# Kernel optimization log

Measured on AMD Instinct MI355X. Metric: run time of the kernel, lower is better.

Reference implementation:

```python
import jax, jax.numpy as jnp
import numpy as np

B, T, D, NH = 4, 2048, 1024, 16
HD = D // NH


def setup_inputs() -> dict:
    key = jax.random.key(0)
    ks = jax.random.split(key, 6)
    scale = 0.02
    x = jax.random.normal(ks[0], (B, T, D), dtype=jnp.float32)
    Wr = jax.random.normal(ks[1], (D, D), dtype=jnp.float32) * scale
    Wk = jax.random.normal(ks[2], (D, D), dtype=jnp.float32) * scale
    Wv = jax.random.normal(ks[3], (D, D), dtype=jnp.float32) * scale
    Ww = jax.random.normal(ks[4], (D, D), dtype=jnp.float32) * scale
    Wo = jax.random.normal(ks[5], (D, D), dtype=jnp.float32) * scale
    return {"x": x, "Wr": Wr, "Wk": Wk, "Wv": Wv, "Ww": Ww, "Wo": Wo}


def _rwkv7_forward(x, Wr, Wk, Wv, Ww, Wo):
    b, t, d = x.shape
    nh, hd = NH, d // NH
    # projections (F.linear: x @ W.T), no bias
    r = jax.nn.sigmoid(x @ Wr.T).reshape(b, t, nh, hd)
    k = (x @ Wk.T).reshape(b, t, nh, hd)
    v = (x @ Wv.T).reshape(b, t, nh, hd)
    w = (jax.nn.sigmoid(x @ Ww.T) * 0.99).reshape(b, t, nh, hd)

    def step(state, inp):
        # state: [B, nh, hd_v, hd_k]
        w_t, k_t, v_t, r_t = inp  # each [B, nh, hd]
        state = state * w_t[..., :, None] + v_t[..., :, None] * k_t[..., None, :]
        out_t = r_t * state.sum(-1)  # [B, nh, hd]
        return state, out_t

    seq = (jnp.moveaxis(w, 1, 0), jnp.moveaxis(k, 1, 0),
           jnp.moveaxis(v, 1, 0), jnp.moveaxis(r, 1, 0))  # time-major
    state0 = jnp.zeros((b, nh, hd, hd), dtype=x.dtype)
    _, outs = jax.lax.scan(step, state0, seq)  # [T, B, nh, hd]
    out = jnp.moveaxis(outs, 0, 1).reshape(b, t, d)

    # RMSNorm with eps=None -> torch uses dtype eps
    eps = jnp.asarray(jnp.finfo(out.dtype).eps, out.dtype)
    out = out * jax.lax.rsqrt(jnp.mean(out * out, axis=-1, keepdims=True) + eps)
    return out @ Wo.T


def reference(x, Wr, Wk, Wv, Ww, Wo):
    return _rwkv7_forward(x, Wr, Wk, Wv, Ww, Wo)
```

## Files before the change

### kernel.cpp

```cpp
#include <hip/hip_runtime.h>
#include <hip/hip_bf16.h>
#include <stdint.h>


#define BB 4
#define TT 2048
#define DD 1024
#define NHH 16
#define HDD 64
#define CC 64
#define LL 32
#define NCH 4096

using bf16 = __hip_bfloat16;
typedef __attribute__((ext_vector_type(8))) short bfrag8;
typedef __attribute__((ext_vector_type(4))) float f32x4;

__device__ __forceinline__ void async_ld16(const bf16* g, bf16* l) {
  __builtin_amdgcn_global_load_lds(
      (const __attribute__((address_space(1))) uint32_t*)g,
      (__attribute__((address_space(3))) uint32_t*)l, 16, 0, 0);
}

__device__ __forceinline__ float sigm(float x) { return 1.0f / (1.0f + expf(-x)); }
__device__ __forceinline__ float bf2f(bf16 h) {
  unsigned short u = *reinterpret_cast<unsigned short*>(&h);
  return __uint_as_float((unsigned)u << 16);
}
__device__ __forceinline__ unsigned short f2bfbits(float f) {
  bf16 b = __float2bfloat16(f);
  return *reinterpret_cast<unsigned short*>(&b);
}

__global__ __launch_bounds__(256)
void convert_kernel(const float* __restrict__ x,
                    const float* __restrict__ Wr, const float* __restrict__ Wv,
                    const float* __restrict__ Ww, const float* __restrict__ Wo,
                    bf16* __restrict__ x_c, bf16* __restrict__ W_c)
{
  const long g = (long)blockIdx.x * 256 + threadIdx.x;
  const float* src; bf16* dst; long off4;
  if (g < 2097152) { src = x; dst = x_c; off4 = g; }
  else {
    long gg = g - 2097152;
    int wsel = (int)(gg >> 18);
    off4 = gg & 262143;
    src = (wsel == 0) ? Wr : (wsel == 1) ? Wv : (wsel == 2) ? Ww : Wo;
    dst = W_c + (long)wsel * 1048576;
  }
  float4 f = reinterpret_cast<const float4*>(src)[off4];
  ushort4 pk;
  pk.x = f2bfbits(f.x); pk.y = f2bfbits(f.y);
  pk.z = f2bfbits(f.z); pk.w = f2bfbits(f.w);
  reinterpret_cast<ushort4*>(dst)[off4] = pk;
}

__global__ __launch_bounds__(256)
void wksum_kernel(const float* __restrict__ Wk, float* __restrict__ wks)
{
  const int gid = blockIdx.x * 256 + threadIdx.x;
  const int h = gid >> 10, c = gid & 1023;
  float s = 0.0f;
  for (int j = 0; j < 64; ++j)
    s += Wk[(long)((h << 6) + j) * 1024 + c];
  wks[gid] = s;
}

__device__ __forceinline__ void gemm_mainloop(
    const bf16* __restrict__ A, const bf16* __restrict__ W,
    int blockM, int blockN, bf16* a_sh, bf16* b_sh, f32x4 acc[4][4])
{
  const int tid    = threadIdx.x;
  const int wave   = tid >> 6;
  const int lane   = tid & 63;
  const int lane15 = lane & 15;
  const int quad   = lane >> 4;
  const int waveM  = wave >> 1;
  const int waveN  = wave & 1;
  const int s_row  = (wave << 5) + (lane >> 2);
  const int s_col  = (((lane & 3) ^ ((lane >> 2) & 3)) << 3);

  const bf16* gA = A + ((long)(blockM * 128) + s_row) * 1024 + s_col;
  const bf16* gW = W + ((long)(blockN * 128) + s_row) * 1024 + s_col;
  bf16* la = a_sh + wave * 1024;
  bf16* lb = b_sh + wave * 1024;

  const int sw = (quad ^ (lane15 & 3)) << 3;

  for (int k0 = 0; k0 < 1024; k0 += 32) {
    async_ld16(gA + k0,            la);
    async_ld16(gA + k0 + 16*1024,  la + 512);
    async_ld16(gW + k0,            lb);
    async_ld16(gW + k0 + 16*1024,  lb + 512);
    __syncthreads();
    bfrag8 af[4], bfv[4];
#pragma unroll
    for (int mi = 0; mi < 4; ++mi)
      af[mi] = *reinterpret_cast<const bfrag8*>(a_sh + (waveM*64 + mi*16 + lane15)*32 + sw);
#pragma unroll
    for (int ni = 0; ni < 4; ++ni)
      bfv[ni] = *reinterpret_cast<const bfrag8*>(b_sh + (waveN*64 + ni*16 + lane15)*32 + sw);
#pragma unroll
    for (int mi = 0; mi < 4; ++mi)
#pragma unroll
      for (int ni = 0; ni < 4; ++ni)
        acc[mi][ni] = __builtin_amdgcn_mfma_f32_16x16x32_bf16(af[mi], bfv[ni], acc[mi][ni], 0, 0, 0);
    __syncthreads();
  }
}

__global__ __launch_bounds__(256, 2)
void proj_kernel(const bf16* __restrict__ X, const bf16* __restrict__ W_c,
                 bf16* __restrict__ r_out, bf16* __restrict__ v_out,
                 bf16* __restrict__ w_out)
{
  __shared__ __align__(16) bf16 a_sh[128*32];
  __shared__ __align__(16) bf16 b_sh[128*32];
  const int f  = blockIdx.x;
  const int u  = f & 7;
  const int q  = f >> 3;
  const int n  = q & 7;
  const int p  = q >> 3;
  const int mh = p & 7;
  const int mode = p >> 3;
  const int m  = u + (mh << 3);

  const bf16* W = W_c + (long)mode * 1048576;
  f32x4 acc[4][4] = {};
  gemm_mainloop(X, W, m, n, a_sh, b_sh, acc);

  const int tid = threadIdx.x;
  const int wave = tid >> 6, lane = tid & 63;
  const int lane15 = lane & 15, quad = lane >> 4;
  const int waveM = wave >> 1, waveN = wave & 1;
  const int m_base = m * 128 + waveM * 64;
  const int n_base = n * 128 + waveN * 64;
  bf16* outp = (mode == 0) ? r_out : (mode == 1) ? v_out : w_out;
#pragma unroll
  for (int mi = 0; mi < 4; ++mi)
#pragma unroll
    for (int ni = 0; ni < 4; ++ni)
#pragma unroll
      for (int r = 0; r < 4; ++r) {
        float val = acc[mi][ni][r];
        if (mode == 0) val = sigm(val);
        else if (mode == 2) val = sigm(val) * 0.99f;
        int mm = m_base + mi*16 + quad*4 + r;
        int nn = n_base + ni*16 + lane15;
        outp[(long)mm * DD + nn] = __float2bfloat16(val);
      }
}

__global__ __launch_bounds__(256)
void ksum_kernel(const bf16* __restrict__ X, const float* __restrict__ wks,
                 float* __restrict__ ksum)
{
  __shared__ __align__(8) bf16 xs[DD];
  const int m = blockIdx.x;
  const int tid = threadIdx.x;
  *reinterpret_cast<ushort4*>(xs + tid*4) =
      *reinterpret_cast<const ushort4*>(X + (long)m * DD + tid*4);
  __syncthreads();
  const int wave = tid >> 6, lane = tid & 63;
  const int b = m >> 11, t = m & (TT - 1);
#pragma unroll
  for (int hi = 0; hi < 4; ++hi) {
    const int h = wave * 4 + hi;
    float acc = 0.0f;
#pragma unroll
    for (int i = 0; i < 16; ++i) {
      const int c = lane + (i << 6);
      acc += bf2f(xs[c]) * wks[h * DD + c];
    }
#pragma unroll
    for (int msk = 1; msk <= 32; msk <<= 1) acc += __shfl_xor(acc, msk);
    if (lane == 0) ksum[((long)(b * NHH + h)) * TT + t] = acc;
  }
}

__global__ __launch_bounds__(256)
void scanA_kernel(const bf16* __restrict__ v_buf, const bf16* __restrict__ w_buf,
                  const float* __restrict__ ksum,
                  float* __restrict__ Pbuf, float* __restrict__ Abuf)
{
  __shared__ float ks_sh[128];
  const int bh = blockIdx.x;
  const int b = bh >> 4, h = bh & 15;
  const int tid = threadIdx.x;
  const int i = tid & 63;
  const int cg = tid >> 6;
  const int chunk = blockIdx.y * 4 + cg;
  if (tid < 128) ks_sh[tid] = ksum[(long)bh * TT + blockIdx.y * 128 + tid];
  __syncthreads();
  const long base = (long)b * TT * DD + (long)(chunk * LL) * DD + h * HDD + i;
  float s = 0.0f, P = 1.0f;
#pragma unroll
  for (int j = 0; j < LL; ++j) {
    const long idx = base + (long)j * DD;
    float wv = bf2f(w_buf[idx]);
    float vv = bf2f(v_buf[idx]);
    s = fmaf(wv, s, vv * ks_sh[cg * LL + j]);
    P *= wv;
  }
  const int ch = bh * 64 + i;
  Pbuf[chunk * NCH + ch] = P;
  Abuf[chunk * NCH + ch] = s;
}

__global__ __launch_bounds__(256)
void scanB_kernel(const float* __restrict__ Pbuf, float* __restrict__ Abuf)
{
  const int ch = blockIdx.x * 256 + threadIdx.x;
  float carry = 0.0f;
  for (int c = 0; c < CC; ++c) {
    const int idx = c * NCH + ch;
    float p = Pbuf[idx];
    float a = Abuf[idx];
    Abuf[idx] = carry;
    carry = fmaf(p, carry, a);
  }
}

__global__ __launch_bounds__(256)
void scanC_kernel(const bf16* __restrict__ r_buf, bf16* v_so,
                  const bf16* __restrict__ w_buf, const float* __restrict__ ksum,
                  const float* __restrict__ Abuf)
{
  __shared__ float ks_sh[128];
  const int bh = blockIdx.x;
  const int b = bh >> 4, h = bh & 15;
  const int tid = threadIdx.x;
  const int i = tid & 63;
  const int cg = tid >> 6;
  const int chunk = blockIdx.y * 4 + cg;
  if (tid < 128) ks_sh[tid] = ksum[(long)bh * TT + blockIdx.y * 128 + tid];
  __syncthreads();
  const int ch = bh * 64 + i;
  const long base = (long)b * TT * DD + (long)(chunk * LL) * DD + h * HDD + i;
  float s = Abuf[chunk * NCH + ch];
#pragma unroll
  for (int j = 0; j < LL; ++j) {
    const long idx = base + (long)j * DD;
    float wv = bf2f(w_buf[idx]);
    float vv = bf2f(v_so[idx]);
    float rv = bf2f(r_buf[idx]);
    s = fmaf(wv, s, vv * ks_sh[cg * LL + j]);
    v_so[idx] = __float2bfloat16(rv * s);
  }
}

__global__ __launch_bounds__(256)
void rmsnorm_inplace(bf16* so)
{
  const long row = blockIdx.x;
  bf16* p = so + row * DD + threadIdx.x * 4;
  ushort4 u = *reinterpret_cast<const ushort4*>(p);
  float x0 = __uint_as_float((unsigned)u.x << 16);
  float x1 = __uint_as_float((unsigned)u.y << 16);
  float x2 = __uint_as_float((unsigned)u.z << 16);
  float x3 = __uint_as_float((unsigned)u.w << 16);
  float ss = x0*x0 + x1*x1 + x2*x2 + x3*x3;
#pragma unroll
  for (int m = 1; m <= 32; m <<= 1) ss += __shfl_xor(ss, m);
  __shared__ float part[4];
  if ((threadIdx.x & 63) == 0) part[threadIdx.x >> 6] = ss;
  __syncthreads();
  const float total = part[0] + part[1] + part[2] + part[3];
  const float scale = rsqrtf(total * (1.0f / DD) + 1.1920929e-07f);
  ushort4 pk;
  pk.x = f2bfbits(x0 * scale); pk.y = f2bfbits(x1 * scale);
  pk.z = f2bfbits(x2 * scale); pk.w = f2bfbits(x3 * scale);
  *reinterpret_cast<ushort4*>(p) = pk;
}

__global__ __launch_bounds__(256, 2)
void out_gemm_kernel(const bf16* __restrict__ A, const bf16* __restrict__ Wo_c,
                     float* __restrict__ out)
{
  __shared__ __align__(16) bf16 a_sh[128*32];
  __shared__ __align__(16) bf16 b_sh[128*32];
  const int f  = blockIdx.x;
  const int u  = f & 7;
  const int q  = f >> 3;
  const int n  = q & 7;
  const int mh = q >> 3;
  const int m  = u + (mh << 3);

  f32x4 acc[4][4] = {};
  gemm_mainloop(A, Wo_c, m, n, a_sh, b_sh, acc);

  const int tid = threadIdx.x;
  const int wave = tid >> 6, lane = tid & 63;
  const int lane15 = lane & 15, quad = lane >> 4;
  const int waveM = wave >> 1, waveN = wave & 1;
  const int m_base = m * 128 + waveM * 64;
  const int n_base = n * 128 + waveN * 64;
#pragma unroll
  for (int mi = 0; mi < 4; ++mi)
#pragma unroll
    for (int ni = 0; ni < 4; ++ni)
#pragma unroll
      for (int r = 0; r < 4; ++r) {
        int mm = m_base + mi*16 + quad*4 + r;
        int nn = n_base + ni*16 + lane15;
        out[(long)mm * DD + nn] = acc[mi][ni][r];
      }
}

extern "C" void kernel_launch(void* const* d_in, const int* in_sizes, int n_in,
                              void* d_out, int out_size, void* d_ws, size_t ws_size,
                              hipStream_t stream) {
  const float* x  = (const float*)d_in[0];
  const float* Wr = (const float*)d_in[1];
  const float* Wk = (const float*)d_in[2];
  const float* Wv = (const float*)d_in[3];
  const float* Ww = (const float*)d_in[4];
  const float* Wo = (const float*)d_in[5];

  const long NELT = (long)BB * TT * DD;
  bf16*  x_c  = (bf16*)d_ws;
  bf16*  W_c  = x_c + NELT;
  bf16*  v_so = W_c + 4 * 1048576;
  float* ksum = (float*)(v_so + NELT);
  float* wks  = ksum + (long)BB * NHH * TT;
  float* Pbuf = wks + NHH * DD;
  float* Abuf = Pbuf + (long)CC * NCH;

  bf16*  r_buf = (bf16*)d_out;
  bf16*  w_buf = (bf16*)d_out + NELT;
  float* out   = (float*)d_out;

  convert_kernel<<<dim3(12288), 256, 0, stream>>>(x, Wr, Wv, Ww, Wo, x_c, W_c);
  wksum_kernel<<<dim3(64), 256, 0, stream>>>(Wk, wks);
  proj_kernel<<<dim3(1536), 256, 0, stream>>>(x_c, W_c, r_buf, v_so, w_buf);
  ksum_kernel<<<dim3(BB * TT), 256, 0, stream>>>(x_c, wks, ksum);
  scanA_kernel<<<dim3(64, 16), 256, 0, stream>>>(v_so, w_buf, ksum, Pbuf, Abuf);
  scanB_kernel<<<dim3(16), 256, 0, stream>>>(Pbuf, Abuf);
  scanC_kernel<<<dim3(64, 16), 256, 0, stream>>>(r_buf, v_so, w_buf, ksum, Abuf);
  rmsnorm_inplace<<<dim3(BB * TT), 256, 0, stream>>>(v_so);
  out_gemm_kernel<<<dim3(512), 256, 0, stream>>>(v_so, W_c + 3 * 1048576, out);
}
```

Before: 266.0 us.

## Double GEMM K-tile to 64, fuse wksum into convert, use fast sigmoid

```diff
diff --git a/kernel.cpp b/kernel.cpp
--- a/kernel.cpp
+++ b/kernel.cpp
@@ -22,7 +22,9 @@
       (__attribute__((address_space(3))) uint32_t*)l, 16, 0, 0);
 }
 
-__device__ __forceinline__ float sigm(float x) { return 1.0f / (1.0f + expf(-x)); }
+__device__ __forceinline__ float sigm(float x) {
+  return __builtin_amdgcn_rcpf(1.0f + __expf(-x));
+}
 __device__ __forceinline__ float bf2f(bf16 h) {
   unsigned short u = *reinterpret_cast<unsigned short*>(&h);
   return __uint_as_float((unsigned)u << 16);
@@ -36,8 +38,19 @@
 void convert_kernel(const float* __restrict__ x,
                     const float* __restrict__ Wr, const float* __restrict__ Wv,
                     const float* __restrict__ Ww, const float* __restrict__ Wo,
-                    bf16* __restrict__ x_c, bf16* __restrict__ W_c)
-{
+                    const float* __restrict__ Wk,
+                    bf16* __restrict__ x_c, bf16* __restrict__ W_c,
+                    float* __restrict__ wks)
+{
+  if (blockIdx.x >= 12288) {
+    const int gid = (blockIdx.x - 12288) * 256 + threadIdx.x;
+    const int h = gid >> 10, c = gid & 1023;
+    float s = 0.0f;
+    for (int j = 0; j < 64; ++j)
+      s += Wk[(long)((h << 6) + j) * 1024 + c];
+    wks[gid] = s;
+    return;
+  }
   const long g = (long)blockIdx.x * 256 + threadIdx.x;
   const float* src; bf16* dst; long off4;
   if (g < 2097152) { src = x; dst = x_c; off4 = g; }
@@ -55,17 +68,6 @@
   reinterpret_cast<ushort4*>(dst)[off4] = pk;
 }
 
-__global__ __launch_bounds__(256)
-void wksum_kernel(const float* __restrict__ Wk, float* __restrict__ wks)
-{
-  const int gid = blockIdx.x * 256 + threadIdx.x;
-  const int h = gid >> 10, c = gid & 1023;
-  float s = 0.0f;
-  for (int j = 0; j < 64; ++j)
-    s += Wk[(long)((h << 6) + j) * 1024 + c];
-  wks[gid] = s;
-}
-
 __device__ __forceinline__ void gemm_mainloop(
     const bf16* __restrict__ A, const bf16* __restrict__ W,
     int blockM, int blockN, bf16* a_sh, bf16* b_sh, f32x4 acc[4][4])
@@ -77,34 +79,39 @@
   const int quad   = lane >> 4;
   const int waveM  = wave >> 1;
   const int waveN  = wave & 1;
-  const int s_row  = (wave << 5) + (lane >> 2);
-  const int s_col  = (((lane & 3) ^ ((lane >> 2) & 3)) << 3);
+  const int s_row  = (wave << 5) + (lane >> 3);
+  const int s_col  = (((lane & 7) ^ ((lane >> 3) & 7)) << 3);
 
   const bf16* gA = A + ((long)(blockM * 128) + s_row) * 1024 + s_col;
   const bf16* gW = W + ((long)(blockN * 128) + s_row) * 1024 + s_col;
-  bf16* la = a_sh + wave * 1024;
-  bf16* lb = b_sh + wave * 1024;
-
-  const int sw = (quad ^ (lane15 & 3)) << 3;
-
-  for (int k0 = 0; k0 < 1024; k0 += 32) {
-    async_ld16(gA + k0,            la);
-    async_ld16(gA + k0 + 16*1024,  la + 512);
-    async_ld16(gW + k0,            lb);
-    async_ld16(gW + k0 + 16*1024,  lb + 512);
+  bf16* la = a_sh + wave * 2048;
+  bf16* lb = b_sh + wave * 2048;
+
+  const int rsw = lane15 & 7;
+
+  for (int k0 = 0; k0 < 1024; k0 += 64) {
+#pragma unroll
+    for (int it = 0; it < 4; ++it) {
+      async_ld16(gA + k0 + it * 8 * 1024, la + it * 512);
+      async_ld16(gW + k0 + it * 8 * 1024, lb + it * 512);
+    }
     __syncthreads();
-    bfrag8 af[4], bfv[4];
-#pragma unroll
-    for (int mi = 0; mi < 4; ++mi)
-      af[mi] = *reinterpret_cast<const bfrag8*>(a_sh + (waveM*64 + mi*16 + lane15)*32 + sw);
-#pragma unroll
-    for (int ni = 0; ni < 4; ++ni)
-      bfv[ni] = *reinterpret_cast<const bfrag8*>(b_sh + (waveN*64 + ni*16 + lane15)*32 + sw);
-#pragma unroll
-    for (int mi = 0; mi < 4; ++mi)
+#pragma unroll
+    for (int kh = 0; kh < 2; ++kh) {
+      bfrag8 af[4], bfv[4];
+      const int pc = ((kh * 4 + quad) ^ rsw) << 3;
+#pragma unroll
+      for (int mi = 0; mi < 4; ++mi)
+        af[mi] = *reinterpret_cast<const bfrag8*>(a_sh + (waveM*64 + mi*16 + lane15)*64 + pc);
 #pragma unroll
       for (int ni = 0; ni < 4; ++ni)
-        acc[mi][ni] = __builtin_amdgcn_mfma_f32_16x16x32_bf16(af[mi], bfv[ni], acc[mi][ni], 0, 0, 0);
+        bfv[ni] = *reinterpret_cast<const bfrag8*>(b_sh + (waveN*64 + ni*16 + lane15)*64 + pc);
+#pragma unroll
+      for (int mi = 0; mi < 4; ++mi)
+#pragma unroll
+        for (int ni = 0; ni < 4; ++ni)
+          acc[mi][ni] = __builtin_amdgcn_mfma_f32_16x16x32_bf16(af[mi], bfv[ni], acc[mi][ni], 0, 0, 0);
+    }
     __syncthreads();
   }
 }
@@ -114,8 +121,8 @@
                  bf16* __restrict__ r_out, bf16* __restrict__ v_out,
                  bf16* __restrict__ w_out)
 {
-  __shared__ __align__(16) bf16 a_sh[128*32];
-  __shared__ __align__(16) bf16 b_sh[128*32];
+  __shared__ __align__(16) bf16 a_sh[128*64];
+  __shared__ __align__(16) bf16 b_sh[128*64];
   const int f  = blockIdx.x;
   const int u  = f & 7;
   const int q  = f >> 3;
@@ -277,8 +284,8 @@
 void out_gemm_kernel(const bf16* __restrict__ A, const bf16* __restrict__ Wo_c,
                      float* __restrict__ out)
 {
-  __shared__ __align__(16) bf16 a_sh[128*32];
-  __shared__ __align__(16) bf16 b_sh[128*32];
+  __shared__ __align__(16) bf16 a_sh[128*64];
+  __shared__ __align__(16) bf16 b_sh[128*64];
   const int f  = blockIdx.x;
   const int u  = f & 7;
   const int q  = f >> 3;
@@ -330,8 +337,7 @@
   bf16*  w_buf = (bf16*)d_out + NELT;
   float* out   = (float*)d_out;
 
-  convert_kernel<<<dim3(12288), 256, 0, stream>>>(x, Wr, Wv, Ww, Wo, x_c, W_c);
-  wksum_kernel<<<dim3(64), 256, 0, stream>>>(Wk, wks);
+  convert_kernel<<<dim3(12352), 256, 0, stream>>>(x, Wr, Wv, Ww, Wo, Wk, x_c, W_c, wks);
   proj_kernel<<<dim3(1536), 256, 0, stream>>>(x_c, W_c, r_buf, v_so, w_buf);
   ksum_kernel<<<dim3(BB * TT), 256, 0, stream>>>(x_c, wks, ksum);
   scanA_kernel<<<dim3(64, 16), 256, 0, stream>>>(v_so, w_buf, ksum, Pbuf, Abuf);
```

After: 228.7 us. -14.0%, faster.
